# Optimization experiments

Hardware: AMD Instinct MI355X
Metric: run time of the kernel (lower is better)

## Reference

```python
import jax, jax.numpy as jnp
import numpy as np

N_NODES = 50000
N_EDGES = 1000000
N_GRAPHS = 256
ORIG = 92
ATOM = 64
NBR = 41
EPS = 1e-5


def _bn_train(h, gamma, beta):
    # BatchNorm1d in training mode: batch stats, biased variance
    mu = h.mean(axis=0)
    var = jnp.var(h, axis=0)
    return (h - mu) * jax.lax.rsqrt(var + EPS) * gamma + beta


def setup_inputs() -> dict:
    key = jax.random.key(0)
    ks = jax.random.split(key, 16)
    inp = {
        "x": jax.random.normal(ks[0], (N_NODES, ORIG), dtype=jnp.float32),
        "edge_attr": jax.random.normal(ks[1], (N_EDGES, NBR), dtype=jnp.float32),
        "lower_f": jax.random.normal(ks[2], (N_NODES, ATOM), dtype=jnp.float32),
        "edge_index": jax.random.randint(ks[3], (2, N_EDGES), 0, N_NODES, dtype=jnp.int32),
        "batch": jnp.sort(jax.random.randint(ks[4], (N_NODES,), 0, N_GRAPHS, dtype=jnp.int32)),
        # params
        "emb_W": jax.random.normal(ks[5], (ORIG, ATOM), dtype=jnp.float32) / np.sqrt(ORIG),
        "emb_b": jnp.zeros((ATOM,), dtype=jnp.float32),
        "fc_W": jax.random.normal(ks[6], (2 * ATOM + NBR, 2 * ATOM), dtype=jnp.float32) / np.sqrt(2 * ATOM + NBR),
        "fc_b": jnp.zeros((2 * ATOM,), dtype=jnp.float32),
        "bn1_g": jnp.ones((2 * ATOM,), dtype=jnp.float32),
        "bn1_b": jnp.zeros((2 * ATOM,), dtype=jnp.float32),
        "bn2_g": jnp.ones((ATOM,), dtype=jnp.float32),
        "bn2_b": jnp.zeros((ATOM,), dtype=jnp.float32),
        "att_W": jax.random.normal(ks[7], (ATOM, 1), dtype=jnp.float32) / np.sqrt(ATOM),
        "att_b": jnp.zeros((1,), dtype=jnp.float32),
        "out_W": jax.random.normal(ks[8], (ATOM, 1), dtype=jnp.float32) / np.sqrt(ATOM),
        "out_b": jnp.zeros((1,), dtype=jnp.float32),
    }
    return inp


def reference(x, edge_attr, lower_f, emb_W, emb_b, fc_W, fc_b, bn1_g, bn1_b,
              bn2_g, bn2_b, att_W, att_b, out_W, out_b, edge_index, batch):
    # embedding + lower-level features
    atom_fea = x @ emb_W + emb_b + lower_f  # [N, ATOM]

    # CGConv: gather endpoints, concat with edge features
    src, dst = edge_index[0], edge_index[1]
    total = jnp.concatenate([atom_fea[src], atom_fea[dst], edge_attr], axis=-1)  # [E, 2A+NBR]
    gated = _bn_train(total @ fc_W + fc_b, bn1_g, bn1_b)  # [E, 2A]
    nbr_filter, nbr_core = gated[:, :ATOM], gated[:, ATOM:]
    msg = jax.nn.sigmoid(nbr_filter) * jax.nn.softplus(nbr_core)  # [E, A]
    summed = jax.ops.segment_sum(msg, src, num_segments=N_NODES)  # [N, A]
    atom_out = _bn_train(summed, bn2_g, bn2_b)

    # SiLU + attentional aggregation per graph
    h = jax.nn.silu(atom_out)  # [N, A]
    logits = (h @ att_W + att_b)[:, 0]  # [N]
    seg_max = jax.ops.segment_max(logits, batch, num_segments=N_GRAPHS)
    e = jnp.exp(logits - seg_max[batch])
    denom = jax.ops.segment_sum(e, batch, num_segments=N_GRAPHS)
    alpha = e / denom[batch]  # [N]
    crys = jax.ops.segment_sum(alpha[:, None] * h, batch, num_segments=N_GRAPHS)  # [G, A]
    crys_fea = crys @ out_W + out_b  # [G, 1]
    return atom_out, crys_fea
```

## Files before the change

### kernel.cpp

```cpp
#include <hip/hip_runtime.h>
#include <math.h>

#define NN 50000
#define NE 1000000
#define NG 256
#define ORIGD 92
#define NBRD 41
#define NSPREAD 32
#define SCAN_B 256

typedef unsigned short u16;
typedef __attribute__((ext_vector_type(8))) short short8;
typedef __attribute__((ext_vector_type(4))) float f32x4;

#define OFF_AFB     0
#define OFF_SUMMED  1600000
#define OFF_WT      4800000
#define OFF_BN1SPR  4812288
#define OFF_BN1SC   4820480
#define OFF_BN2ACC  4820736
#define OFF_BN2SC   4820864
#define OFF_ELOG    4820992
#define OFF_SEGMAX  4870992
#define OFF_DENOM   4871248
#define OFF_CNT     4871504
#define OFF_PTR     4921504
#define OFF_HEAD    4971504
#define OFF_BSUM    5021504
#define OFF_BOFS    5021760
#define OFF_SLOT    5022016
#define OFF_H       6022016
#define OFF_T2_END  70022016
#define OFF_EAB     70022016
#define OFF_T3_END  94022016

__device__ __forceinline__ u16 f2b(float f) {
    unsigned u = __float_as_uint(f);
    return (u16)((u + 0x7FFFu + ((u >> 16) & 1u)) >> 16);
}
__device__ __forceinline__ float b2f(u16 u) {
    return __uint_as_float(((unsigned)u) << 16);
}

__global__ __launch_bounds__(256) void k_embed(
    const float* __restrict__ x, const float* __restrict__ lf,
    const float* __restrict__ W, const float* __restrict__ b,
    u16* __restrict__ afb)
{
    int gid = blockIdx.x * 256 + threadIdx.x;
    int n = gid >> 6, c = gid & 63;
    const float* xr = x + (long)n * ORIGD;
    float acc = b[c] + lf[gid];
#pragma unroll 4
    for (int k = 0; k < ORIGD; k++)
        acc = fmaf(xr[k], W[k * 64 + c], acc);
    afb[gid] = f2b(acc);
}

__global__ void k_prepw(const float* __restrict__ fcW, u16* __restrict__ wT)
{
    int i = blockIdx.x * 256 + threadIdx.x;
    int j = i / 192, k = i - j * 192;
    wT[i] = (k < 169) ? f2b(fcW[k * 128 + j]) : (u16)0;
}

__global__ void k_prepea(const float* __restrict__ ea, u16* __restrict__ eab)
{
    int gid = blockIdx.x * 256 + threadIdx.x;
    int e = gid / 48, c = gid - e * 48;
    eab[gid] = (c < NBRD) ? f2b(ea[(long)e * NBRD + c]) : (u16)0;
}

__global__ void k_hist(const int* __restrict__ ei, int* __restrict__ cnt)
{
    int e = blockIdx.x * 256 + threadIdx.x;
    if (e < NE) atomicAdd(&cnt[ei[e]], 1);
}

__global__ void k_partial(const int* __restrict__ cnt, int* __restrict__ lofs,
                          int* __restrict__ bsum)
{
    __shared__ int sd[SCAN_B];
    int t = threadIdx.x, b = blockIdx.x, n = b * SCAN_B + t;
    int v = (n < NN) ? cnt[n] : 0;
    sd[t] = v; __syncthreads();
    for (int o = 1; o < SCAN_B; o <<= 1) {
        int x = (t >= o) ? sd[t - o] : 0;
        __syncthreads();
        sd[t] += x;
        __syncthreads();
    }
    if (n < NN) lofs[n] = sd[t] - v;
    if (t == SCAN_B - 1) bsum[b] = sd[t];
}

__global__ void k_scanb(const int* __restrict__ bsum, int* __restrict__ bofs, int nb)
{
    __shared__ int sd[256];
    int t = threadIdx.x;
    int v = (t < nb) ? bsum[t] : 0;
    sd[t] = v; __syncthreads();
    for (int o = 1; o < 256; o <<= 1) {
        int x = (t >= o) ? sd[t - o] : 0;
        __syncthreads();
        sd[t] += x;
        __syncthreads();
    }
    bofs[t] = sd[t] - v;
}

__global__ void k_addofs(int* __restrict__ ptr, const int* __restrict__ bofs,
                         int* __restrict__ head)
{
    int n = blockIdx.x * 256 + threadIdx.x;
    if (n < NN) {
        int p = ptr[n] + bofs[n >> 8];
        ptr[n] = p; head[n] = p;
    }
}

__global__ void k_slot(const int* __restrict__ ei, int* __restrict__ head,
                       int* __restrict__ slot)
{
    int e = blockIdx.x * 256 + threadIdx.x;
    if (e < NE) slot[e] = atomicAdd(&head[ei[e]], 1);
}

template <int EAB>
__global__ __launch_bounds__(256) void k_gemm_h(
    const u16* __restrict__ afb, const float* __restrict__ ea,
    const u16* __restrict__ eab, const int* __restrict__ ei,
    const int* __restrict__ slot, const u16* __restrict__ wT,
    u16* __restrict__ h, float* __restrict__ spread)
{
    __shared__ __align__(16) u16 sTl[64 * 200];
    __shared__ int sSrc[64], sDst[64], sSlot[64];
    const int tid = threadIdx.x;
    const int e0 = blockIdx.x * 64;

    if (tid < 64) sSrc[tid] = ei[e0 + tid];
    else if (tid < 128) sDst[tid - 64] = ei[NE + e0 + tid - 64];
    else if (tid < 192) sSlot[tid - 128] = slot[e0 + tid - 128];
    __syncthreads();

    for (int i = tid; i < 1024; i += 256) {
        int e = i >> 4, q = i & 15;
        const u16* g = (q < 8) ? (afb + (long)sSrc[e] * 64 + q * 8)
                               : (afb + (long)sDst[e] * 64 + (q - 8) * 8);
        *(short8*)(sTl + e * 200 + q * 8) = *(const short8*)g;
    }
    if (EAB) {
        for (int i = tid; i < 512; i += 256) {
            if (i < 384) {
                int e = i / 6, q = i - e * 6;
                *(short8*)(sTl + e * 200 + 128 + q * 8) =
                    *(const short8*)(eab + (long)(e0 + e) * 48 + q * 8);
            } else {
                int j = i - 384; int e = j >> 1, q = j & 1;
                short8 z = {0,0,0,0,0,0,0,0};
                *(short8*)(sTl + e * 200 + 176 + q * 8) = z;
            }
        }
    } else {
        for (int i = tid; i < 64 * 64; i += 256) {
            int e = i >> 6, c = i & 63;
            float v = (c < NBRD) ? ea[(long)(e0 + e) * NBRD + c] : 0.f;
            sTl[e * 200 + 128 + c] = f2b(v);
        }
    }
    __syncthreads();

    const int lane = tid & 63, w = tid >> 6;
    const int n16 = lane & 15, quad = lane >> 4;

    short8 A0[6], A1[6];
    {
        const u16* b0 = wT + (16 * w + n16) * 192 + quad * 8;
        const u16* b1 = wT + (16 * (w + 4) + n16) * 192 + quad * 8;
#pragma unroll
        for (int ks = 0; ks < 6; ks++) {
            A0[ks] = *(const short8*)(b0 + ks * 32);
            A1[ks] = *(const short8*)(b1 + ks * 32);
        }
    }

    const int j0 = 16 * w + 4 * quad;
    float s0[4] = {0,0,0,0}, q0[4] = {0,0,0,0}, s1[4] = {0,0,0,0}, q1[4] = {0,0,0,0};

    for (int t = 0; t < 4; t++) {
        const u16* row = sTl + (16 * t + n16) * 200 + quad * 8;
        f32x4 acc0 = {0.f, 0.f, 0.f, 0.f}, acc1 = {0.f, 0.f, 0.f, 0.f};
#pragma unroll
        for (int ks = 0; ks < 6; ks++) {
            short8 b = *(const short8*)(row + ks * 32);
            acc0 = __builtin_amdgcn_mfma_f32_16x16x32_bf16(A0[ks], b, acc0, 0, 0, 0);
            acc1 = __builtin_amdgcn_mfma_f32_16x16x32_bf16(A1[ks], b, acc1, 0, 0, 0);
        }
#pragma unroll
        for (int r = 0; r < 4; r++) {
            s0[r] += acc0[r]; q0[r] = fmaf(acc0[r], acc0[r], q0[r]);
            s1[r] += acc1[r]; q1[r] = fmaf(acc1[r], acc1[r], q1[r]);
        }
        u16* hp = h + (long)sSlot[16 * t + n16] * 128 + j0;
        ushort4 v0 = make_ushort4(f2b(acc0[0]), f2b(acc0[1]), f2b(acc0[2]), f2b(acc0[3]));
        ushort4 v1 = make_ushort4(f2b(acc1[0]), f2b(acc1[1]), f2b(acc1[2]), f2b(acc1[3]));
        *(ushort4*)hp = v0;
        *(ushort4*)(hp + 64) = v1;
    }

#pragma unroll
    for (int m = 1; m < 16; m <<= 1) {
#pragma unroll
        for (int r = 0; r < 4; r++) {
            s0[r] += __shfl_xor(s0[r], m); q0[r] += __shfl_xor(q0[r], m);
            s1[r] += __shfl_xor(s1[r], m); q1[r] += __shfl_xor(q1[r], m);
        }
    }
    if (n16 == 0) {
        float* sp = spread + (blockIdx.x & (NSPREAD - 1)) * 256;
#pragma unroll
        for (int r = 0; r < 4; r++) {
            atomicAdd(sp + j0 + r,       s0[r]);
            atomicAdd(sp + 128 + j0 + r, q0[r]);
            atomicAdd(sp + 64 + j0 + r,  s1[r]);
            atomicAdd(sp + 192 + j0 + r, q1[r]);
        }
    }
}

template <int MODE>
__global__ __launch_bounds__(256) void k_gemm(
    const u16* __restrict__ afb, const float* __restrict__ ea,
    const int* __restrict__ ei, const u16* __restrict__ wT,
    const float* __restrict__ sc, float* __restrict__ outbuf)
{
    __shared__ __align__(16) u16 sTl[64 * 200];
    __shared__ int sSrc[64], sDst[64];
    const int tid = threadIdx.x;
    const int e0 = blockIdx.x * 64;

    if (tid < 64) sSrc[tid] = ei[e0 + tid];
    else if (tid < 128) sDst[tid - 64] = ei[NE + e0 + tid - 64];
    __syncthreads();
    for (int i = tid; i < 1024; i += 256) {
        int e = i >> 4, q = i & 15;
        const u16* g = (q < 8) ? (afb + (long)sSrc[e] * 64 + q * 8)
                               : (afb + (long)sDst[e] * 64 + (q - 8) * 8);
        *(short8*)(sTl + e * 200 + q * 8) = *(const short8*)g;
    }
    for (int i = tid; i < 64 * 64; i += 256) {
        int e = i >> 6, c = i & 63;
        float v = (c < NBRD) ? ea[(long)(e0 + e) * NBRD + c] : 0.f;
        sTl[e * 200 + 128 + c] = f2b(v);
    }
    __syncthreads();

    const int lane = tid & 63, w = tid >> 6;
    const int n16 = lane & 15, quad = lane >> 4;
    short8 A0[6], A1[6];
    {
        const u16* b0 = wT + (16 * w + n16) * 192 + quad * 8;
        const u16* b1 = wT + (16 * (w + 4) + n16) * 192 + quad * 8;
#pragma unroll
        for (int ks = 0; ks < 6; ks++) {
            A0[ks] = *(const short8*)(b0 + ks * 32);
            A1[ks] = *(const short8*)(b1 + ks * 32);
        }
    }
    const int j0 = 16 * w + 4 * quad;
    float s0[4] = {0,0,0,0}, q0[4] = {0,0,0,0}, s1[4] = {0,0,0,0}, q1[4] = {0,0,0,0};
    float scf[4], shf[4], scc[4], shc[4];
    if (MODE == 1) {
#pragma unroll
        for (int r = 0; r < 4; r++) {
            scf[r] = sc[j0 + r];        shf[r] = sc[128 + j0 + r];
            scc[r] = sc[64 + j0 + r];   shc[r] = sc[192 + j0 + r];
        }
    }
    for (int t = 0; t < 4; t++) {
        const u16* row = sTl + (16 * t + n16) * 200 + quad * 8;
        f32x4 acc0 = {0.f, 0.f, 0.f, 0.f}, acc1 = {0.f, 0.f, 0.f, 0.f};
#pragma unroll
        for (int ks = 0; ks < 6; ks++) {
            short8 b = *(const short8*)(row + ks * 32);
            acc0 = __builtin_amdgcn_mfma_f32_16x16x32_bf16(A0[ks], b, acc0, 0, 0, 0);
            acc1 = __builtin_amdgcn_mfma_f32_16x16x32_bf16(A1[ks], b, acc1, 0, 0, 0);
        }
        if (MODE == 0) {
#pragma unroll
            for (int r = 0; r < 4; r++) {
                s0[r] += acc0[r]; q0[r] = fmaf(acc0[r], acc0[r], q0[r]);
                s1[r] += acc1[r]; q1[r] = fmaf(acc1[r], acc1[r], q1[r]);
            }
        } else {
            int src = sSrc[16 * t + n16];
            float* dst = outbuf + (long)src * 64 + j0;
#pragma unroll
            for (int r = 0; r < 4; r++) {
                float f  = fmaf(acc0[r], scf[r], shf[r]);
                float cc = fmaf(acc1[r], scc[r], shc[r]);
                float sig = 1.f / (1.f + expf(-f));
                float sp  = fmaxf(cc, 0.f) + log1pf(expf(-fabsf(cc)));
                atomicAdd(dst + r, sig * sp);
            }
        }
    }
    if (MODE == 0) {
#pragma unroll
        for (int m = 1; m < 16; m <<= 1) {
#pragma unroll
            for (int r = 0; r < 4; r++) {
                s0[r] += __shfl_xor(s0[r], m); q0[r] += __shfl_xor(q0[r], m);
                s1[r] += __shfl_xor(s1[r], m); q1[r] += __shfl_xor(q1[r], m);
            }
        }
        if (n16 == 0) {
            float* sp = outbuf + (blockIdx.x & (NSPREAD - 1)) * 256;
#pragma unroll
            for (int r = 0; r < 4; r++) {
                atomicAdd(sp + j0 + r,       s0[r]);
                atomicAdd(sp + 128 + j0 + r, q0[r]);
                atomicAdd(sp + 64 + j0 + r,  s1[r]);
                atomicAdd(sp + 192 + j0 + r, q1[r]);
            }
        }
    }
}

__global__ void k_bn1fin(const float* __restrict__ spread,
                         const float* __restrict__ g, const float* __restrict__ b,
                         float* __restrict__ sc)
{
    int c = threadIdx.x;
    float s = 0.f, q = 0.f;
    for (int k = 0; k < NSPREAD; k++) { s += spread[k * 256 + c]; q += spread[k * 256 + 128 + c]; }
    float mean_acc = s / (float)NE;
    float var = q / (float)NE - mean_acc * mean_acc;
    float scale = g[c] * rsqrtf(var + 1e-5f);
    sc[c] = scale;
    sc[128 + c] = b[c] - mean_acc * scale;
}

__global__ __launch_bounds__(256) void k_scatter(
    const u16* __restrict__ h, const int* __restrict__ ptr,
    const int* __restrict__ cnt, const float* __restrict__ sc,
    float* __restrict__ summed)
{
    int tid = threadIdx.x;
    int n = blockIdx.x * 4 + (tid >> 6);
    int l = tid & 63;
    int es = l & 7, cg = l >> 3;

    float4 a0 = *(const float4*)(sc + cg * 8);
    float4 a1 = *(const float4*)(sc + cg * 8 + 4);
    float4 b0 = *(const float4*)(sc + 128 + cg * 8);
    float4 b1 = *(const float4*)(sc + 128 + cg * 8 + 4);
    float4 c0 = *(const float4*)(sc + 64 + cg * 8);
    float4 c1 = *(const float4*)(sc + 64 + cg * 8 + 4);
    float4 d0 = *(const float4*)(sc + 192 + cg * 8);
    float4 d1 = *(const float4*)(sc + 192 + cg * 8 + 4);
    float scf[8] = {a0.x,a0.y,a0.z,a0.w,a1.x,a1.y,a1.z,a1.w};
    float shf[8] = {b0.x,b0.y,b0.z,b0.w,b1.x,b1.y,b1.z,b1.w};
    float scc[8] = {c0.x,c0.y,c0.z,c0.w,c1.x,c1.y,c1.z,c1.w};
    float shc[8] = {d0.x,d0.y,d0.z,d0.w,d1.x,d1.y,d1.z,d1.w};

    int p0 = ptr[n], deg = cnt[n];
    float acc[8] = {0,0,0,0,0,0,0,0};
    for (int i = 0; i < deg; i += 8) {
        int idx = i + es;
        bool valid = idx < deg;
        long r = p0 + (valid ? idx : 0);
        const u16* hr = h + r * 128;
        short8 f8 = *(const short8*)(hr + cg * 8);
        short8 c8 = *(const short8*)(hr + 64 + cg * 8);
#pragma unroll
        for (int j = 0; j < 8; j++) {
            float f  = fmaf(b2f((u16)f8[j]), scf[j], shf[j]);
            float cc = fmaf(b2f((u16)c8[j]), scc[j], shc[j]);
            float sig = 1.f / (1.f + expf(-f));
            float sp  = fmaxf(cc, 0.f) + log1pf(expf(-fabsf(cc)));
            acc[j] += valid ? sig * sp : 0.f;
        }
    }
#pragma unroll
    for (int m = 1; m < 8; m <<= 1)
#pragma unroll
        for (int j = 0; j < 8; j++) acc[j] += __shfl_xor(acc[j], m);
    if (es == 0) {
        float* sp = summed + (long)n * 64 + cg * 8;
        float4 v0 = {acc[0], acc[1], acc[2], acc[3]};
        float4 v1 = {acc[4], acc[5], acc[6], acc[7]};
        *(float4*)sp = v0;
        *(float4*)(sp + 4) = v1;
    }
}

__global__ __launch_bounds__(256) void k_bn2stats(const float* __restrict__ summed,
                                                  float* __restrict__ acc2)
{
    int tid = threadIdx.x; int c = tid & 63; int sub = tid >> 6;
    float s = 0.f, q = 0.f;
    for (int r = blockIdx.x * 4 + sub; r < NN; r += 4 * 128) {
        float v = summed[(long)r * 64 + c]; s += v; q = fmaf(v, v, q);
    }
    __shared__ float rs[256], rq[256];
    rs[tid] = s; rq[tid] = q; __syncthreads();
    if (tid < 64) {
        s = rs[tid] + rs[tid + 64] + rs[tid + 128] + rs[tid + 192];
        q = rq[tid] + rq[tid + 64] + rq[tid + 128] + rq[tid + 192];
        atomicAdd(&acc2[tid], s);
        atomicAdd(&acc2[64 + tid], q);
    }
}

__global__ void k_bn2fin(const float* __restrict__ acc2,
                         const float* __restrict__ g, const float* __restrict__ b,
                         float* __restrict__ sc2, const float* __restrict__ outb,
                         float* __restrict__ out)
{
    int c = threadIdx.x;
    if (c < 64) {
        float mean = acc2[c] / (float)NN;
        float var = acc2[64 + c] / (float)NN - mean * mean;
        float scale = g[c] * rsqrtf(var + 1e-5f);
        sc2[c] = scale;
        sc2[64 + c] = b[c] - mean * scale;
    }
    out[(long)NN * 64 + c] = outb[0];
}

__global__ __launch_bounds__(256) void k_nodepost(
    const float* __restrict__ summed, const float* __restrict__ sc2,
    const float* __restrict__ attW, const float* __restrict__ attb,
    const int* __restrict__ batch, float* __restrict__ out,
    float* __restrict__ elog, unsigned* __restrict__ segmax)
{
    int tid = threadIdx.x; int n = blockIdx.x * 4 + (tid >> 6); int c = tid & 63;
    float v = summed[(long)n * 64 + c];
    float ao = fmaf(v, sc2[c], sc2[64 + c]);
    out[(long)n * 64 + c] = ao;
    float h = ao / (1.f + expf(-ao));
    float p = h * attW[c];
#pragma unroll
    for (int off = 32; off; off >>= 1) p += __shfl_down(p, off, 64);
    if (c == 0) {
        float logit = p + attb[0];
        elog[n] = logit;
        unsigned u = __float_as_uint(logit);
        u = (u & 0x80000000u) ? ~u : (u | 0x80000000u);
        atomicMax(&segmax[batch[n]], u);
    }
}

__global__ void k_denom(const int* __restrict__ batch,
                        const unsigned* __restrict__ segmax,
                        float* __restrict__ elog, float* __restrict__ denom)
{
    int n = blockIdx.x * 256 + threadIdx.x;
    if (n >= NN) return;
    int b = batch[n];
    unsigned u = segmax[b];
    u = (u & 0x80000000u) ? (u & 0x7FFFFFFFu) : ~u;
    float e = expf(elog[n] - __uint_as_float(u));
    elog[n] = e;
    atomicAdd(&denom[b], e);
}

__global__ __launch_bounds__(256) void k_crys(
    const float* __restrict__ atom_out, const float* __restrict__ elog,
    const float* __restrict__ denom, const int* __restrict__ batch,
    const float* __restrict__ outW, float* __restrict__ out)
{
    int tid = threadIdx.x; int n = blockIdx.x * 4 + (tid >> 6); int l = tid & 63;
    int b = batch[n];
    float alpha = elog[n] / denom[b];
    float ao = atom_out[(long)n * 64 + l];
    float h = ao / (1.f + expf(-ao));
    float p = h * outW[l];
#pragma unroll
    for (int off = 32; off; off >>= 1) p += __shfl_down(p, off, 64);
    if (l == 0) atomicAdd(&out[(long)NN * 64 + b], alpha * p);
}

extern "C" void kernel_launch(void* const* d_in, const int* in_sizes, int n_in,
                              void* d_out, int out_size, void* d_ws, size_t ws_size,
                              hipStream_t stream)
{
    const float* x    = (const float*)d_in[0];
    const float* eatt = (const float*)d_in[1];
    const float* lf   = (const float*)d_in[2];
    const int*   ei   = (const int*)d_in[3];
    const int*   batch= (const int*)d_in[4];
    const float* embW = (const float*)d_in[5];
    const float* embB = (const float*)d_in[6];
    const float* fcW  = (const float*)d_in[7];
    const float* bn1g = (const float*)d_in[9];
    const float* bn1b = (const float*)d_in[10];
    const float* bn2g = (const float*)d_in[11];
    const float* bn2b = (const float*)d_in[12];
    const float* attW = (const float*)d_in[13];
    const float* attB = (const float*)d_in[14];
    const float* outW = (const float*)d_in[15];
    const float* outB = (const float*)d_in[16];
    float* out = (float*)d_out;
    float* ws  = (float*)d_ws;

    u16* afb  = (u16*)(ws + OFF_AFB);
    u16* wT   = (u16*)(ws + OFF_WT);
    int* cnt  = (int*)(ws + OFF_CNT);
    int* ptr  = (int*)(ws + OFF_PTR);
    int* head = (int*)(ws + OFF_HEAD);
    int* bsum = (int*)(ws + OFF_BSUM);
    int* bofs = (int*)(ws + OFF_BOFS);
    int* slot = (int*)(ws + OFF_SLOT);
    u16* h    = (u16*)(ws + OFF_H);
    u16* eab  = (u16*)(ws + OFF_EAB);

    const bool t3 = ws_size >= (size_t)OFF_T3_END * sizeof(float);
    const bool t2 = ws_size >= (size_t)OFF_T2_END * sizeof(float);

    k_embed<<<12500, 256, 0, stream>>>(x, lf, embW, embB, afb);
    k_prepw<<<96, 256, 0, stream>>>(fcW, wT);

    if (t2) {
        hipMemsetAsync(ws + OFF_BN1SPR, 0,
                       (size_t)(OFF_PTR - OFF_BN1SPR) * sizeof(float), stream);
        if (t3) k_prepea<<<NE * 48 / 256, 256, 0, stream>>>(eatt, eab);
        k_hist<<<(NE + 255) / 256, 256, 0, stream>>>(ei, cnt);
        k_partial<<<(NN + SCAN_B - 1) / SCAN_B, SCAN_B, 0, stream>>>(cnt, ptr, bsum);
        k_scanb<<<1, 256, 0, stream>>>(bsum, bofs, (NN + SCAN_B - 1) / SCAN_B);
        k_addofs<<<(NN + 255) / 256, 256, 0, stream>>>(ptr, bofs, head);
        k_slot<<<(NE + 255) / 256, 256, 0, stream>>>(ei, head, slot);
        if (t3)
            k_gemm_h<1><<<NE / 64, 256, 0, stream>>>(afb, eatt, eab, ei, slot, wT,
                                                     h, ws + OFF_BN1SPR);
        else
            k_gemm_h<0><<<NE / 64, 256, 0, stream>>>(afb, eatt, eab, ei, slot, wT,
                                                     h, ws + OFF_BN1SPR);
        k_bn1fin<<<1, 128, 0, stream>>>(ws + OFF_BN1SPR, bn1g, bn1b, ws + OFF_BN1SC);
        k_scatter<<<NN / 4, 256, 0, stream>>>(h, ptr, cnt, ws + OFF_BN1SC,
                                              ws + OFF_SUMMED);
    } else {
        hipMemsetAsync(ws + OFF_SUMMED, 0,
                       (size_t)(OFF_PTR - OFF_SUMMED) * sizeof(float), stream);
        k_gemm<0><<<NE / 64, 256, 0, stream>>>(afb, eatt, ei, wT, ws + OFF_BN1SC,
                                               ws + OFF_BN1SPR);
        k_bn1fin<<<1, 128, 0, stream>>>(ws + OFF_BN1SPR, bn1g, bn1b, ws + OFF_BN1SC);
        k_gemm<1><<<NE / 64, 256, 0, stream>>>(afb, eatt, ei, wT, ws + OFF_BN1SC,
                                               ws + OFF_SUMMED);
    }

    k_bn2stats<<<128, 256, 0, stream>>>(ws + OFF_SUMMED, ws + OFF_BN2ACC);
    k_bn2fin<<<1, 256, 0, stream>>>(ws + OFF_BN2ACC, bn2g, bn2b, ws + OFF_BN2SC,
                                    outB, out);
    k_nodepost<<<12500, 256, 0, stream>>>(ws + OFF_SUMMED, ws + OFF_BN2SC, attW, attB,
                                          batch, out, ws + OFF_ELOG,
                                          (unsigned*)(ws + OFF_SEGMAX));
    k_denom<<<196, 256, 0, stream>>>(batch, (const unsigned*)(ws + OFF_SEGMAX),
                                     ws + OFF_ELOG, ws + OFF_DENOM);
    k_crys<<<12500, 256, 0, stream>>>(out, ws + OFF_ELOG, ws + OFF_DENOM, batch,
                                      outW, out);
}
```

Measured before the change: 1.396 ms.

## Write GEMM output in edge order and gather via CSR edge index; use fast math

The GEMM kernel now writes h rows contiguously in edge order instead of scattering them to CSR slots. The scatter kernel then reads each edge's row indirectly through a new edge-index array built by a fill kernel. The bf16 edge-attribute pre-conversion pass is removed, so the GEMM always reads fp32 edge features directly. Sigmoid, softplus and SiLU switch to fast intrinsics (__expf, __logf, rcp), which trades some accuracy for cheaper transcendental math and makes the scatter's reads of h random instead of sequential.

```diff
diff --git a/kernel.cpp b/kernel.cpp
--- a/kernel.cpp
+++ b/kernel.cpp
@@ -28,11 +28,9 @@
 #define OFF_HEAD    4971504
 #define OFF_BSUM    5021504
 #define OFF_BOFS    5021760
-#define OFF_SLOT    5022016
+#define OFF_EIDX    5022016
 #define OFF_H       6022016
 #define OFF_T2_END  70022016
-#define OFF_EAB     70022016
-#define OFF_T3_END  94022016
 
 __device__ __forceinline__ u16 f2b(float f) {
     unsigned u = __float_as_uint(f);
@@ -40,6 +38,14 @@
 }
 __device__ __forceinline__ float b2f(u16 u) {
     return __uint_as_float(((unsigned)u) << 16);
+}
+__device__ __forceinline__ float gate(float f, float cc) {
+    float sig = __builtin_amdgcn_rcpf(1.f + __expf(-f));
+    float sp  = fmaxf(cc, 0.f) + __logf(1.f + __expf(-fabsf(cc)));
+    return sig * sp;
+}
+__device__ __forceinline__ float fsilu(float x) {
+    return x * __builtin_amdgcn_rcpf(1.f + __expf(-x));
 }
 
 __global__ __launch_bounds__(256) void k_embed(
@@ -62,13 +68,6 @@
     int i = blockIdx.x * 256 + threadIdx.x;
     int j = i / 192, k = i - j * 192;
     wT[i] = (k < 169) ? f2b(fcW[k * 128 + j]) : (u16)0;
-}
-
-__global__ void k_prepea(const float* __restrict__ ea, u16* __restrict__ eab)
-{
-    int gid = blockIdx.x * 256 + threadIdx.x;
-    int e = gid / 48, c = gid - e * 48;
-    eab[gid] = (c < NBRD) ? f2b(ea[(long)e * NBRD + c]) : (u16)0;
 }
 
 __global__ void k_hist(const int* __restrict__ ei, int* __restrict__ cnt)
@@ -119,28 +118,28 @@
     }
 }
 
-__global__ void k_slot(const int* __restrict__ ei, int* __restrict__ head,
-                       int* __restrict__ slot)
+__global__ void k_fill(const int* __restrict__ ei, int* __restrict__ head,
+                       int* __restrict__ eidx)
 {
     int e = blockIdx.x * 256 + threadIdx.x;
-    if (e < NE) slot[e] = atomicAdd(&head[ei[e]], 1);
-}
-
-template <int EAB>
+    if (e < NE) {
+        int pos = atomicAdd(&head[ei[e]], 1);
+        eidx[pos] = e;
+    }
+}
+
 __global__ __launch_bounds__(256) void k_gemm_h(
     const u16* __restrict__ afb, const float* __restrict__ ea,
-    const u16* __restrict__ eab, const int* __restrict__ ei,
-    const int* __restrict__ slot, const u16* __restrict__ wT,
+    const int* __restrict__ ei, const u16* __restrict__ wT,
     u16* __restrict__ h, float* __restrict__ spread)
 {
     __shared__ __align__(16) u16 sTl[64 * 200];
-    __shared__ int sSrc[64], sDst[64], sSlot[64];
+    __shared__ int sSrc[64], sDst[64];
     const int tid = threadIdx.x;
     const int e0 = blockIdx.x * 64;
 
     if (tid < 64) sSrc[tid] = ei[e0 + tid];
     else if (tid < 128) sDst[tid - 64] = ei[NE + e0 + tid - 64];
-    else if (tid < 192) sSlot[tid - 128] = slot[e0 + tid - 128];
     __syncthreads();
 
     for (int i = tid; i < 1024; i += 256) {
@@ -149,24 +148,10 @@
                                : (afb + (long)sDst[e] * 64 + (q - 8) * 8);
         *(short8*)(sTl + e * 200 + q * 8) = *(const short8*)g;
     }
-    if (EAB) {
-        for (int i = tid; i < 512; i += 256) {
-            if (i < 384) {
-                int e = i / 6, q = i - e * 6;
-                *(short8*)(sTl + e * 200 + 128 + q * 8) =
-                    *(const short8*)(eab + (long)(e0 + e) * 48 + q * 8);
-            } else {
-                int j = i - 384; int e = j >> 1, q = j & 1;
-                short8 z = {0,0,0,0,0,0,0,0};
-                *(short8*)(sTl + e * 200 + 176 + q * 8) = z;
-            }
-        }
-    } else {
-        for (int i = tid; i < 64 * 64; i += 256) {
-            int e = i >> 6, c = i & 63;
-            float v = (c < NBRD) ? ea[(long)(e0 + e) * NBRD + c] : 0.f;
-            sTl[e * 200 + 128 + c] = f2b(v);
-        }
+    for (int i = tid; i < 64 * 64; i += 256) {
+        int e = i >> 6, c = i & 63;
+        float v = (c < NBRD) ? ea[(long)(e0 + e) * NBRD + c] : 0.f;
+        sTl[e * 200 + 128 + c] = f2b(v);
     }
     __syncthreads();
 
@@ -201,7 +186,8 @@
             s0[r] += acc0[r]; q0[r] = fmaf(acc0[r], acc0[r], q0[r]);
             s1[r] += acc1[r]; q1[r] = fmaf(acc1[r], acc1[r], q1[r]);
         }
-        u16* hp = h + (long)sSlot[16 * t + n16] * 128 + j0;
+        int ge = e0 + 16 * t + n16;
+        u16* hp = h + (long)ge * 128 + j0;
         ushort4 v0 = make_ushort4(f2b(acc0[0]), f2b(acc0[1]), f2b(acc0[2]), f2b(acc0[3]));
         ushort4 v1 = make_ushort4(f2b(acc1[0]), f2b(acc1[1]), f2b(acc1[2]), f2b(acc1[3]));
         *(ushort4*)hp = v0;
@@ -299,9 +285,7 @@
             for (int r = 0; r < 4; r++) {
                 float f  = fmaf(acc0[r], scf[r], shf[r]);
                 float cc = fmaf(acc1[r], scc[r], shc[r]);
-                float sig = 1.f / (1.f + expf(-f));
-                float sp  = fmaxf(cc, 0.f) + log1pf(expf(-fabsf(cc)));
-                atomicAdd(dst + r, sig * sp);
+                atomicAdd(dst + r, gate(f, cc));
             }
         }
     }
@@ -343,8 +327,8 @@
 
 __global__ __launch_bounds__(256) void k_scatter(
     const u16* __restrict__ h, const int* __restrict__ ptr,
-    const int* __restrict__ cnt, const float* __restrict__ sc,
-    float* __restrict__ summed)
+    const int* __restrict__ cnt, const int* __restrict__ eidx,
+    const float* __restrict__ sc, float* __restrict__ summed)
 {
     int tid = threadIdx.x;
     int n = blockIdx.x * 4 + (tid >> 6);
@@ -369,17 +353,16 @@
     for (int i = 0; i < deg; i += 8) {
         int idx = i + es;
         bool valid = idx < deg;
-        long r = p0 + (valid ? idx : 0);
-        const u16* hr = h + r * 128;
+        int e = eidx[p0 + (valid ? idx : 0)];
+        const u16* hr = h + (long)e * 128;
         short8 f8 = *(const short8*)(hr + cg * 8);
         short8 c8 = *(const short8*)(hr + 64 + cg * 8);
 #pragma unroll
         for (int j = 0; j < 8; j++) {
             float f  = fmaf(b2f((u16)f8[j]), scf[j], shf[j]);
             float cc = fmaf(b2f((u16)c8[j]), scc[j], shc[j]);
-            float sig = 1.f / (1.f + expf(-f));
-            float sp  = fmaxf(cc, 0.f) + log1pf(expf(-fabsf(cc)));
-            acc[j] += valid ? sig * sp : 0.f;
+            float g  = gate(f, cc);
+            acc[j] += valid ? g : 0.f;
         }
     }
 #pragma unroll
@@ -439,7 +422,7 @@
     float v = summed[(long)n * 64 + c];
     float ao = fmaf(v, sc2[c], sc2[64 + c]);
     out[(long)n * 64 + c] = ao;
-    float h = ao / (1.f + expf(-ao));
+    float h = fsilu(ao);
     float p = h * attW[c];
 #pragma unroll
     for (int off = 32; off; off >>= 1) p += __shfl_down(p, off, 64);
@@ -461,7 +444,7 @@
     int b = batch[n];
     unsigned u = segmax[b];
     u = (u & 0x80000000u) ? (u & 0x7FFFFFFFu) : ~u;
-    float e = expf(elog[n] - __uint_as_float(u));
+    float e = __expf(elog[n] - __uint_as_float(u));
     elog[n] = e;
     atomicAdd(&denom[b], e);
 }
@@ -475,8 +458,7 @@
     int b = batch[n];
     float alpha = elog[n] / denom[b];
     float ao = atom_out[(long)n * 64 + l];
-    float h = ao / (1.f + expf(-ao));
-    float p = h * outW[l];
+    float p = fsilu(ao) * outW[l];
 #pragma unroll
     for (int off = 32; off; off >>= 1) p += __shfl_down(p, off, 64);
     if (l == 0) atomicAdd(&out[(long)NN * 64 + b], alpha * p);
@@ -512,11 +494,9 @@
     int* head = (int*)(ws + OFF_HEAD);
     int* bsum = (int*)(ws + OFF_BSUM);
     int* bofs = (int*)(ws + OFF_BOFS);
-    int* slot = (int*)(ws + OFF_SLOT);
+    int* eidx = (int*)(ws + OFF_EIDX);
     u16* h    = (u16*)(ws + OFF_H);
-    u16* eab  = (u16*)(ws + OFF_EAB);
-
-    const bool t3 = ws_size >= (size_t)OFF_T3_END * sizeof(float);
+
     const bool t2 = ws_size >= (size_t)OFF_T2_END * sizeof(float);
 
     k_embed<<<12500, 256, 0, stream>>>(x, lf, embW, embB, afb);
@@ -525,20 +505,14 @@
     if (t2) {
         hipMemsetAsync(ws + OFF_BN1SPR, 0,
                        (size_t)(OFF_PTR - OFF_BN1SPR) * sizeof(float), stream);
-        if (t3) k_prepea<<<NE * 48 / 256, 256, 0, stream>>>(eatt, eab);
         k_hist<<<(NE + 255) / 256, 256, 0, stream>>>(ei, cnt);
         k_partial<<<(NN + SCAN_B - 1) / SCAN_B, SCAN_B, 0, stream>>>(cnt, ptr, bsum);
         k_scanb<<<1, 256, 0, stream>>>(bsum, bofs, (NN + SCAN_B - 1) / SCAN_B);
         k_addofs<<<(NN + 255) / 256, 256, 0, stream>>>(ptr, bofs, head);
-        k_slot<<<(NE + 255) / 256, 256, 0, stream>>>(ei, head, slot);
-        if (t3)
-            k_gemm_h<1><<<NE / 64, 256, 0, stream>>>(afb, eatt, eab, ei, slot, wT,
-                                                     h, ws + OFF_BN1SPR);
-        else
-            k_gemm_h<0><<<NE / 64, 256, 0, stream>>>(afb, eatt, eab, ei, slot, wT,
-                                                     h, ws + OFF_BN1SPR);
+        k_fill<<<(NE + 255) / 256, 256, 0, stream>>>(ei, head, eidx);
+        k_gemm_h<<<NE / 64, 256, 0, stream>>>(afb, eatt, ei, wT, h, ws + OFF_BN1SPR);
         k_bn1fin<<<1, 128, 0, stream>>>(ws + OFF_BN1SPR, bn1g, bn1b, ws + OFF_BN1SC);
-        k_scatter<<<NN / 4, 256, 0, stream>>>(h, ptr, cnt, ws + OFF_BN1SC,
+        k_scatter<<<NN / 4, 256, 0, stream>>>(h, ptr, cnt, eidx, ws + OFF_BN1SC,
                                               ws + OFF_SUMMED);
     } else {
         hipMemsetAsync(ws + OFF_SUMMED, 0,
```

New measurement: 1.205 ms. 1.16x faster.
